# Kernel optimization log

Hardware: AMD Instinct MI355X
Metric: run time of the kernel (lower is better)

The kernel has to match this reference:

```python
import jax, jax.numpy as jnp
import numpy as np

BETA = 0.25  # commitment loss weight (beta)
EPS_NORM = 1e-12  # F.normalize eps


def l2norm(t):
    return t / jnp.clip(jnp.linalg.norm(t, axis=-1, keepdims=True), EPS_NORM)


def setup_inputs() -> dict:
    key = jax.random.key(0)
    k1, k2 = jax.random.split(key)
    z = jax.random.normal(k1, (16, 256, 32, 32), dtype=jnp.float32)
    # EmbeddingEMA with kmeans_init=False: weight = l2norm(randn(n_embed, dim))
    weight = l2norm(jax.random.normal(k2, (8192, 256), dtype=jnp.float32))
    return {"z": z, "weight": weight}


def reference(z, weight):
    # z: [B, C, H, W] -> [B, H, W, C], l2-normalized per token
    zc = l2norm(jnp.transpose(z, (0, 2, 3, 1)))
    B, H, W, D = zc.shape
    zf = zc.reshape(-1, D)  # [N, D]
    zf_d = jax.lax.stop_gradient(zf)
    # negative squared L2 distance: -|z|^2 - |w|^2 + 2 z.w  -> argmax = nearest code
    d = (-jnp.sum(zf_d ** 2, axis=1, keepdims=True)
         - jnp.sum(weight ** 2, axis=1)
         + 2.0 * jnp.einsum('nd,kd->nk', zf_d, weight))  # [N, K]
    idx = jnp.argmax(d, axis=1)  # [N]
    z_q = weight[idx].reshape(B, H, W, D)  # codebook gather
    # commitment loss: beta * mean((sg(z_q) - z)^2)
    loss = BETA * jnp.mean((jax.lax.stop_gradient(z_q) - zc) ** 2)
    # straight-through estimator
    z_q = zc + jax.lax.stop_gradient(z_q - zc)
    z_q = jnp.transpose(z_q, (0, 3, 1, 2))  # back to [B, C, H, W]
    return z_q, loss, idx
```

## Files before the change

kernel.cpp:

```cpp
#include <hip/hip_runtime.h>
#include <math.h>

#define BB   16
#define CC   256
#define HW   1024
#define NN   16384
#define DD   256
#define KK   8192
#define ZQ_SIZE 4194304
#define MARGIN 0.017f
#define GCAP 8192
#define RSPLIT 8

typedef __attribute__((ext_vector_type(8))) short short8;
typedef __attribute__((ext_vector_type(4))) float f32x4;

static __device__ inline unsigned short f2bf(float x) {
    unsigned int u = __float_as_uint(x);
    unsigned int r = (u + 0x7fff + ((u >> 16) & 1)) >> 16;
    return (unsigned short)r;
}

static __device__ inline unsigned long long pack_key(float s, int k) {
    unsigned int bits = __float_as_uint(s);
    unsigned int o = (bits & 0x80000000u) ? ~bits : (bits | 0x80000000u);
    return ((unsigned long long)o << 32) | (unsigned int)(~k);
}

__global__ __launch_bounds__(256) void wsqwb_kernel(const float* __restrict__ W,
                                                    float* __restrict__ wsq,
                                                    unsigned short* __restrict__ wb,
                                                    int* __restrict__ gcnt,
                                                    int* __restrict__ oflow) {
    if (blockIdx.x == 0) {
        gcnt[threadIdx.x] = 0;
        if (threadIdx.x == 0) *oflow = 0;
    }
    {
        const int lane = threadIdx.x & 63;
        const int k = blockIdx.x * 4 + (threadIdx.x >> 6);
        float4 v = *(const float4*)(W + (size_t)k * DD + lane * 4);
        float s = v.x * v.x + v.y * v.y + v.z * v.z + v.w * v.w;
        #pragma unroll
        for (int off = 32; off; off >>= 1) s += __shfl_down(s, off);
        if (lane == 0) wsq[k] = s;
    }
    if (blockIdx.x < 1024) {
        const int ch = blockIdx.x * 256 + threadIdx.x;
        const int c = (ch >> 7) & 7;
        const int r = ch & 127;
        const int kt = ch >> 12, dc = (ch >> 10) & 3;
        const int k = kt * 128 + r;
        const int d0 = dc * 64 + c * 8;
        const float4 v0 = *(const float4*)(W + (size_t)k * DD + d0);
        const float4 v1 = *(const float4*)(W + (size_t)k * DD + d0 + 4);
        uint4 out;
        out.x = (unsigned int)f2bf(v0.x) | ((unsigned int)f2bf(v0.y) << 16);
        out.y = (unsigned int)f2bf(v0.z) | ((unsigned int)f2bf(v0.w) << 16);
        out.z = (unsigned int)f2bf(v1.x) | ((unsigned int)f2bf(v1.y) << 16);
        out.w = (unsigned int)f2bf(v1.z) | ((unsigned int)f2bf(v1.w) << 16);
        *(uint4*)(wb + (size_t)ch * 8) = out;
    }
}

__global__ __launch_bounds__(256) void normalize_kernel(const float* __restrict__ z,
                                                        float* __restrict__ zn,
                                                        float* __restrict__ znsq,
                                                        unsigned short* __restrict__ zb) {
    __shared__ float tile[64][257];
    __shared__ float s_nrm[64];
    const int t   = threadIdx.x;
    const int b   = blockIdx.x >> 4;
    const int hw0 = (blockIdx.x & 15) * 64;

    #pragma unroll
    for (int cg = 0; cg < 16; ++cg) {
        int c  = cg * 16 + (t >> 4);
        int hw = (t & 15) * 4;
        float4 v = *(const float4*)(z + ((size_t)(b * CC + c) << 10) + hw0 + hw);
        tile[hw + 0][c] = v.x;
        tile[hw + 1][c] = v.y;
        tile[hw + 2][c] = v.z;
        tile[hw + 3][c] = v.w;
    }
    __syncthreads();
    if (t < 64) {
        float s = 0.f;
        #pragma unroll 8
        for (int c = 0; c < 256; ++c) { float v = tile[t][c]; s += v * v; }
        float nrm = sqrtf(s);
        nrm = fmaxf(nrm, 1e-12f);
        s_nrm[t] = nrm;
        znsq[(size_t)b * HW + hw0 + t] = s / (nrm * nrm);
    }
    __syncthreads();
    const int n0 = b * HW + hw0;
    for (int r = 0; r < 64; ++r) {
        zn[(size_t)(n0 + r) * DD + t] = tile[r][t] / s_nrm[r];
    }
    const int r    = t & 63;
    const int mt   = n0 >> 7;
    const int rg   = (n0 & 127) + r;
    const float nrm = s_nrm[r];
    #pragma unroll
    for (int loop = 0; loop < 8; ++loop) {
        int comb = loop * 4 + (t >> 6);
        int dc = comb >> 3, c = comb & 7;
        int d0 = dc * 64 + c * 8;
        uint4 out;
        out.x = (unsigned int)f2bf(tile[r][d0 + 0] / nrm) | ((unsigned int)f2bf(tile[r][d0 + 1] / nrm) << 16);
        out.y = (unsigned int)f2bf(tile[r][d0 + 2] / nrm) | ((unsigned int)f2bf(tile[r][d0 + 3] / nrm) << 16);
        out.z = (unsigned int)f2bf(tile[r][d0 + 4] / nrm) | ((unsigned int)f2bf(tile[r][d0 + 5] / nrm) << 16);
        out.w = (unsigned int)f2bf(tile[r][d0 + 6] / nrm) | ((unsigned int)f2bf(tile[r][d0 + 7] / nrm) << 16);
        *(uint4*)(zb + (size_t)(mt * 4 + dc) * 8192 + (size_t)(c * 128 + rg) * 8) = out;
    }
}

__global__ __launch_bounds__(256) void score_kernel(const unsigned short* __restrict__ zb,
                                                    const unsigned short* __restrict__ wb,
                                                    const float* __restrict__ wsqv,
                                                    float* __restrict__ cmax) {
    __shared__ unsigned short sA[8192];
    __shared__ unsigned short sB[8192];
    __shared__ float rowbuf[128][4];
    __shared__ __align__(16) float swsq[128];

    const int tid  = threadIdx.x;
    const int w    = tid >> 6;
    const int lane = tid & 63;
    const int wcr  = w >> 1;
    const int wct  = w & 1;
    const int q    = lane >> 4, c15 = lane & 15;
    const int kt   = blockIdx.x & 63;
    const int mt   = blockIdx.x >> 6;

    if (tid < 128) swsq[tid] = wsqv[kt * 128 + tid];

    f32x4 acc[4][4];
    #pragma unroll
    for (int fi = 0; fi < 4; ++fi)
        #pragma unroll
        for (int fj = 0; fj < 4; ++fj)
            acc[fi][fj] = (f32x4){0.f, 0.f, 0.f, 0.f};

    for (int dc = 0; dc < 4; ++dc) {
        const unsigned short* gA = zb + (size_t)(mt * 4 + dc) * 8192;
        const unsigned short* gB = wb + (size_t)(kt * 4 + dc) * 8192;
        #pragma unroll
        for (int i = 0; i < 4; ++i) {
            int eo = ((w * 4 + i) << 9);
            __builtin_amdgcn_global_load_lds(
                (const __attribute__((address_space(1))) void*)(gA + eo + lane * 8),
                (__attribute__((address_space(3))) void*)(sA + eo), 16, 0, 0);
            __builtin_amdgcn_global_load_lds(
                (const __attribute__((address_space(1))) void*)(gB + eo + lane * 8),
                (__attribute__((address_space(3))) void*)(sB + eo), 16, 0, 0);
        }
        __syncthreads();
        #pragma unroll
        for (int ks = 0; ks < 2; ++ks) {
            short8 tfr[4], cfr[4];
            const int ca = (ks * 4 + q) * 128;
            #pragma unroll
            for (int f = 0; f < 4; ++f) {
                tfr[f] = *(const short8*)(sA + (size_t)(ca + wct * 64 + f * 16 + c15) * 8);
                cfr[f] = *(const short8*)(sB + (size_t)(ca + wcr * 64 + f * 16 + c15) * 8);
            }
            #pragma unroll
            for (int fi = 0; fi < 4; ++fi)
                #pragma unroll
                for (int fj = 0; fj < 4; ++fj)
                    acc[fi][fj] = __builtin_amdgcn_mfma_f32_16x16x32_bf16(
                        cfr[fi], tfr[fj], acc[fi][fj], 0, 0, 0);
        }
        __syncthreads();
    }

    f32x4 wq4[4];
    #pragma unroll
    for (int fi = 0; fi < 4; ++fi)
        wq4[fi] = *(const f32x4*)(&swsq[wcr * 64 + fi * 16 + q * 4]);

    #pragma unroll
    for (int fj = 0; fj < 4; ++fj) {
        float g[2];
        #pragma unroll
        for (int p = 0; p < 2; ++p) {
            float vm = -INFINITY;
            #pragma unroll
            for (int f2 = 0; f2 < 2; ++f2) {
                int fi = p * 2 + f2;
                #pragma unroll
                for (int rg = 0; rg < 4; ++rg)
                    vm = fmaxf(vm, 2.0f * acc[fi][fj][rg] - wq4[fi][rg]);
            }
            vm = fmaxf(vm, __shfl_xor(vm, 16));
            vm = fmaxf(vm, __shfl_xor(vm, 32));
            g[p] = vm;
        }
        if (q == 0) {
            int row = wct * 64 + fj * 16 + c15;
            rowbuf[row][wcr * 2 + 0] = g[0];
            rowbuf[row][wcr * 2 + 1] = g[1];
        }
    }
    __syncthreads();
    {
        int row = tid >> 1, half = tid & 1;
        float2 v2 = make_float2(rowbuf[row][half * 2], rowbuf[row][half * 2 + 1]);
        *(float2*)(cmax + (size_t)(mt * 128 + row) * 256 + kt * 4 + half * 2) = v2;
    }
}

__global__ __launch_bounds__(256) void cand_kernel(const float* __restrict__ cmax,
                                                   unsigned int* __restrict__ gseg,
                                                   int* __restrict__ gcnt,
                                                   unsigned long long* __restrict__ packed,
                                                   int* __restrict__ nflag,
                                                   int* __restrict__ oflow) {
    const int t = threadIdx.x, wv = t >> 6, lane = t & 63;
    const int n = blockIdx.x * 4 + wv;
    float4 c4 = *(const float4*)(cmax + (size_t)n * 256 + lane * 4);
    float lm = fmaxf(fmaxf(c4.x, c4.y), fmaxf(c4.z, c4.w));
    #pragma unroll
    for (int off = 1; off <= 32; off <<= 1) lm = fmaxf(lm, __shfl_xor(lm, off));
    const float thresh = lm - MARGIN;
    if (lane == 0) { packed[n] = 0ull; nflag[n] = 0; }
    float g4[4] = {c4.x, c4.y, c4.z, c4.w};
    #pragma unroll
    for (int j = 0; j < 4; ++j) {
        int g = lane * 4 + j;
        if (g4[j] >= thresh) {
            int pos = atomicAdd(&gcnt[g], 1);
            if (pos < GCAP) gseg[(size_t)g * GCAP + pos] = (unsigned int)n;
            else { nflag[n] = 1; atomicAdd(oflow, 1); }
        }
    }
}

__global__ __launch_bounds__(256) void rescore_kernel(const float* __restrict__ zn,
                                                      const float* __restrict__ W,
                                                      const float* __restrict__ wsqv,
                                                      const float* __restrict__ znsq,
                                                      const unsigned int* __restrict__ gseg,
                                                      const int* __restrict__ gcnt,
                                                      unsigned long long* __restrict__ packed) {
    __shared__ float sW[32 * 260];
    __shared__ float znr[4][2][256];

    const int t = threadIdx.x;
    const int g   = blockIdx.x >> 3;
    const int sub = blockIdx.x & 7;
    int cnt = gcnt[g]; if (cnt > GCAP) cnt = GCAP;
    if (cnt <= sub * 8) return;

    {
        int c = t >> 3, i = t & 7;
        const float4* src = (const float4*)(W + (size_t)g * 8192 + c * 256 + i * 32);
        #pragma unroll
        for (int j = 0; j < 8; ++j)
            *(float4*)(sW + c * 260 + i * 32 + j * 4) = src[j];
    }
    __syncthreads();

    const int wv = t >> 6, lane = t & 63;
    const int h = lane >> 5, c = lane & 31;
    const int k = g * 32 + c;
    const float wq = wsqv[k];
    const float4* wrow = (const float4*)(sW + c * 260);

    for (int base = (sub * 4 + wv) * 2; base < cnt; base += RSPLIT * 8) {
        int idx = base + h; if (idx >= cnt) idx = base;
        int n = (int)gseg[(size_t)g * GCAP + idx];
        *(float4*)(&znr[wv][h][c * 8])     = *(const float4*)(zn + (size_t)n * DD + c * 8);
        *(float4*)(&znr[wv][h][c * 8 + 4]) = *(const float4*)(zn + (size_t)n * DD + c * 8 + 4);
        float d = 0.f;
        #pragma unroll
        for (int j = 0; j < 64; ++j) {
            float4 wv4 = wrow[j];
            float4 zv  = *(const float4*)(&znr[wv][h][j * 4]);
            d += wv4.x * zv.x + wv4.y * zv.y + wv4.z * zv.z + wv4.w * zv.w;
        }
        float s = (-znsq[n] - wq) + 2.0f * d;
        unsigned long long key = pack_key(s, k);
        #pragma unroll
        for (int off = 1; off <= 16; off <<= 1) {
            unsigned long long ok = __shfl_xor(key, off);
            if (ok > key) key = ok;
        }
        if (c == 0) atomicMax(packed + n, key);
    }
}

__global__ __launch_bounds__(256) void fullscan_kernel(const float* __restrict__ zn,
                                                       const float* __restrict__ W,
                                                       const float* __restrict__ wsqv,
                                                       const float* __restrict__ znsq,
                                                       const int* __restrict__ nflag,
                                                       const int* __restrict__ oflow,
                                                       unsigned long long* __restrict__ packed) {
    if (*oflow == 0) return;
    const int t = threadIdx.x, wv = t >> 6, lane = t & 63;
    const int code = lane >> 1, part = lane & 1;
    for (int n = blockIdx.x * 4 + wv; n < NN; n += gridDim.x * 4) {
        if (!nflag[n]) continue;
        float zsq = znsq[n];
        unsigned long long best = 0ull;
        for (int gg = 0; gg < 256; ++gg) {
            int k = gg * 32 + code;
            const float4* wrp = (const float4*)(W + (size_t)k * DD + part * 128);
            const float4* zrp = (const float4*)(zn + (size_t)n * DD + part * 128);
            float d = 0.f;
            #pragma unroll
            for (int jj = 0; jj < 32; ++jj) {
                float4 a = zrp[jj], b = wrp[jj];
                d += a.x * b.x + a.y * b.y + a.z * b.z + a.w * b.w;
            }
            d += __shfl_xor(d, 1);
            unsigned long long key = pack_key((-zsq - wsqv[k]) + 2.0f * d, k);
            if (key > best) best = key;
        }
        #pragma unroll
        for (int off = 1; off <= 32; off <<= 1) {
            unsigned long long ok = __shfl_xor(best, off);
            if (ok > best) best = ok;
        }
        if (lane == 0) atomicMax(packed + n, best);
    }
}

__global__ __launch_bounds__(256) void gatherfin_kernel(const float* __restrict__ W,
                                                        const unsigned long long* __restrict__ packed,
                                                        float* __restrict__ idxf,
                                                        float* __restrict__ partials,
                                                        float* __restrict__ zq) {
    __shared__ int sbk[64];
    const int t   = threadIdx.x;
    const int b   = blockIdx.x >> 4;
    const int hw0 = (blockIdx.x & 15) * 64;
    if (t < 64) {
        int n = b * HW + hw0 + t;
        unsigned long long key = packed[n];
        int k = (int)((~(unsigned int)key) & 0x3FFFu);
        unsigned int o = (unsigned int)(key >> 32);
        unsigned int bits = (o & 0x80000000u) ? (o & 0x7FFFFFFFu) : ~o;
        float s = __uint_as_float(bits);
        sbk[t] = k;
        idxf[n] = (float)k;
        float cc = -s;
        #pragma unroll
        for (int off = 32; off; off >>= 1) cc += __shfl_down(cc, off);
        if (t == 0) partials[blockIdx.x] = cc;
    }
    __syncthreads();
    const int hw  = t & 63;
    const int c0  = (t >> 6) * 4;
    const int row = sbk[hw];
    #pragma unroll
    for (int cg = 0; cg < 16; ++cg) {
        int c = cg * 16 + c0;
        float4 v = *(const float4*)(W + (size_t)row * DD + c);
        size_t base = ((size_t)(b * CC + c) << 10) + hw0 + hw;
        zq[base]        = v.x;
        zq[base + 1024] = v.y;
        zq[base + 2048] = v.z;
        zq[base + 3072] = v.w;
    }
}

__global__ __launch_bounds__(256) void loss_final_kernel(const float* __restrict__ partials,
                                                         float* __restrict__ out_loss) {
    __shared__ float wsum[4];
    const int t = threadIdx.x;
    float v = partials[t];
    #pragma unroll
    for (int off = 32; off; off >>= 1) v += __shfl_down(v, off);
    if ((t & 63) == 0) wsum[t >> 6] = v;
    __syncthreads();
    if (t == 0) {
        float tot = wsum[0] + wsum[1] + wsum[2] + wsum[3];
        *out_loss = 0.25f * (tot / (float)ZQ_SIZE);
    }
}

extern "C" void kernel_launch(void* const* d_in, const int* in_sizes, int n_in,
                              void* d_out, int out_size, void* d_ws, size_t ws_size,
                              hipStream_t stream) {
    const float* z = (const float*)d_in[0];
    const float* W = (const float*)d_in[1];

    float* out   = (float*)d_out;
    float* zq    = out;
    float* loss  = out + ZQ_SIZE;
    float* idxf  = out + ZQ_SIZE + 1;

    float* ws       = (float*)d_ws;
    float* zn       = ws;
    float* znsq     = zn + (size_t)NN * DD;
    float* wsqv     = znsq + NN;
    float* partials = wsqv + KK;
    int*   gcnt     = (int*)(partials + 256);
    int*   oflow    = gcnt + 256;
    int*   nflag    = oflow + 64;
    unsigned short* zb = (unsigned short*)(nflag + NN);
    unsigned short* wb = zb + (size_t)NN * DD;
    float* cmax     = (float*)(wb + (size_t)KK * DD);
    unsigned int* gseg = (unsigned int*)(cmax + (size_t)NN * 256);
    unsigned long long* packed = (unsigned long long*)(gseg + (size_t)256 * GCAP);

    wsqwb_kernel     <<<KK / 4, 256, 0, stream>>>(W, wsqv, wb, gcnt, oflow);
    normalize_kernel <<<BB * 16, 256, 0, stream>>>(z, zn, znsq, zb);
    score_kernel     <<<(NN / 128) * (KK / 128), 256, 0, stream>>>(zb, wb, wsqv, cmax);
    cand_kernel      <<<NN / 4, 256, 0, stream>>>(cmax, gseg, gcnt, packed, nflag, oflow);
    rescore_kernel   <<<256 * RSPLIT, 256, 0, stream>>>(zn, W, wsqv, znsq, gseg, gcnt, packed);
    fullscan_kernel  <<<64, 256, 0, stream>>>(zn, W, wsqv, znsq, nflag, oflow, packed);
    gatherfin_kernel <<<BB * 16, 256, 0, stream>>>(W, packed, idxf, partials, zq);
    loss_final_kernel<<<1, 256, 0, stream>>>(partials, loss);
}
```

Measured before the change: 233.4 us.

## Enlarge score GEMM tiles to 256x256 with double-buffered LDS staging

The bf16 scoring GEMM moves from 128x128 tiles with 256 threads to 256x256 tiles with 512 threads. Loads go through double-buffered global-to-LDS staging, with explicit vmcnt waits so the next d-chunk loads while the current one is computed. MFMA sections are wrapped in barriers and s_setprio. The larger tile halves global reloads of both operands, and the output per block becomes a group max over 32 codes, the same granularity as before. In exchange it uses about 128KB of LDS and more accumulator registers per block, which lowers occupancy.

New measurement: 238.3 us. +2.1%, slower.

```diff
diff --git a/kernel.cpp b/kernel.cpp
--- a/kernel.cpp
+++ b/kernel.cpp
@@ -116,99 +116,130 @@
     }
 }
 
-__global__ __launch_bounds__(256) void score_kernel(const unsigned short* __restrict__ zb,
-                                                    const unsigned short* __restrict__ wb,
-                                                    const float* __restrict__ wsqv,
-                                                    float* __restrict__ cmax) {
-    __shared__ unsigned short sA[8192];
-    __shared__ unsigned short sB[8192];
-    __shared__ float rowbuf[128][4];
-    __shared__ __align__(16) float swsq[128];
+__global__ __launch_bounds__(512, 2) void score_kernel(const unsigned short* __restrict__ zb,
+                                                       const unsigned short* __restrict__ wb,
+                                                       const float* __restrict__ wsqv,
+                                                       float* __restrict__ cmax) {
+    __shared__ __align__(16) unsigned short sT[2][16384];
+    __shared__ __align__(16) unsigned short sC[2][16384];
+    __shared__ float rowbuf[8][260];
+    __shared__ __align__(16) float swsq[256];
 
     const int tid  = threadIdx.x;
     const int w    = tid >> 6;
     const int lane = tid & 63;
-    const int wcr  = w >> 1;
-    const int wct  = w & 1;
+    const int wr   = w >> 2;
+    const int wc   = w & 3;
     const int q    = lane >> 4, c15 = lane & 15;
-    const int kt   = blockIdx.x & 63;
-    const int mt   = blockIdx.x >> 6;
-
-    if (tid < 128) swsq[tid] = wsqv[kt * 128 + tid];
-
-    f32x4 acc[4][4];
-    #pragma unroll
-    for (int fi = 0; fi < 4; ++fi)
+    const int kt   = blockIdx.x & 31;
+    const int mt   = blockIdx.x >> 5;
+    const int mtb  = mt * 8;
+    const int ktb  = kt * 8;
+
+    if (tid < 256) swsq[tid] = wsqv[kt * 256 + tid];
+
+    const int sh = (w >> 1) & 1;
+    auto stage = [&](int bf, int dc) {
+        const unsigned short* gs = (w < 4)
+            ? (zb + (size_t)(mtb + sh * 4 + dc) * 8192)
+            : (wb + (size_t)(ktb + sh * 4 + dc) * 8192);
+        unsigned short* ld = (w < 4) ? &sT[bf][sh * 8192] : &sC[bf][sh * 8192];
+        #pragma unroll
+        for (int i = 0; i < 8; ++i) {
+            const int eo = ((w & 1) * 8 + i) << 9;
+            __builtin_amdgcn_global_load_lds(
+                (const __attribute__((address_space(1))) void*)(gs + eo + lane * 8),
+                (__attribute__((address_space(3))) void*)(ld + eo), 16, 0, 0);
+        }
+    };
+
+    f32x4 acc[8][4];
+    #pragma unroll
+    for (int fi = 0; fi < 8; ++fi)
         #pragma unroll
         for (int fj = 0; fj < 4; ++fj)
             acc[fi][fj] = (f32x4){0.f, 0.f, 0.f, 0.f};
 
-    for (int dc = 0; dc < 4; ++dc) {
-        const unsigned short* gA = zb + (size_t)(mt * 4 + dc) * 8192;
-        const unsigned short* gB = wb + (size_t)(kt * 4 + dc) * 8192;
-        #pragma unroll
-        for (int i = 0; i < 4; ++i) {
-            int eo = ((w * 4 + i) << 9);
-            __builtin_amdgcn_global_load_lds(
-                (const __attribute__((address_space(1))) void*)(gA + eo + lane * 8),
-                (__attribute__((address_space(3))) void*)(sA + eo), 16, 0, 0);
-            __builtin_amdgcn_global_load_lds(
-                (const __attribute__((address_space(1))) void*)(gB + eo + lane * 8),
-                (__attribute__((address_space(3))) void*)(sB + eo), 16, 0, 0);
-        }
-        __syncthreads();
+    const int tHalf = wc >> 1;
+    const int tRow0 = (wc & 1) * 64 + c15;
+
+    stage(0, 0);
+    stage(1, 1);
+    asm volatile("s_waitcnt vmcnt(8)" ::: "memory");
+    __builtin_amdgcn_s_barrier();
+
+    #pragma unroll
+    for (int t = 0; t < 4; ++t) {
+        const int bf = t & 1;
+        const unsigned short* sTb = &sT[bf][tHalf * 8192];
+        const unsigned short* sCb = &sC[bf][wr * 8192];
         #pragma unroll
         for (int ks = 0; ks < 2; ++ks) {
-            short8 tfr[4], cfr[4];
             const int ca = (ks * 4 + q) * 128;
+            short8 tfr[4];
             #pragma unroll
-            for (int f = 0; f < 4; ++f) {
-                tfr[f] = *(const short8*)(sA + (size_t)(ca + wct * 64 + f * 16 + c15) * 8);
-                cfr[f] = *(const short8*)(sB + (size_t)(ca + wcr * 64 + f * 16 + c15) * 8);
+            for (int fj = 0; fj < 4; ++fj)
+                tfr[fj] = *(const short8*)(sTb + (size_t)(ca + tRow0 + fj * 16) * 8);
+            #pragma unroll
+            for (int fih = 0; fih < 2; ++fih) {
+                short8 cfr[4];
+                #pragma unroll
+                for (int f = 0; f < 4; ++f)
+                    cfr[f] = *(const short8*)(sCb + (size_t)(ca + fih * 64 + f * 16 + c15) * 8);
+                __builtin_amdgcn_s_barrier();
+                __builtin_amdgcn_s_setprio(1);
+                #pragma unroll
+                for (int f = 0; f < 4; ++f)
+                    #pragma unroll
+                    for (int fj = 0; fj < 4; ++fj)
+                        acc[fih * 4 + f][fj] = __builtin_amdgcn_mfma_f32_16x16x32_bf16(
+                            cfr[f], tfr[fj], acc[fih * 4 + f][fj], 0, 0, 0);
+                __builtin_amdgcn_s_setprio(0);
+                __builtin_amdgcn_s_barrier();
             }
-            #pragma unroll
-            for (int fi = 0; fi < 4; ++fi)
-                #pragma unroll
-                for (int fj = 0; fj < 4; ++fj)
-                    acc[fi][fj] = __builtin_amdgcn_mfma_f32_16x16x32_bf16(
-                        cfr[fi], tfr[fj], acc[fi][fj], 0, 0, 0);
-        }
-        __syncthreads();
-    }
-
-    f32x4 wq4[4];
-    #pragma unroll
-    for (int fi = 0; fi < 4; ++fi)
-        wq4[fi] = *(const f32x4*)(&swsq[wcr * 64 + fi * 16 + q * 4]);
+        }
+        asm volatile("s_waitcnt lgkmcnt(0)" ::: "memory");
+        __builtin_amdgcn_s_barrier();
+        if (t == 0)      { stage(0, 2); asm volatile("s_waitcnt vmcnt(8)" ::: "memory"); }
+        else if (t == 1) { stage(1, 3); asm volatile("s_waitcnt vmcnt(8)" ::: "memory"); }
+        else if (t == 2) {              asm volatile("s_waitcnt vmcnt(0)" ::: "memory"); }
+        __builtin_amdgcn_s_barrier();
+    }
+
+    f32x4 wq4[8];
+    #pragma unroll
+    for (int fi = 0; fi < 8; ++fi)
+        wq4[fi] = *(const f32x4*)(&swsq[wr * 128 + fi * 16 + q * 4]);
 
     #pragma unroll
     for (int fj = 0; fj < 4; ++fj) {
-        float g[2];
-        #pragma unroll
-        for (int p = 0; p < 2; ++p) {
-            float vm = -INFINITY;
+        float vg[4];
+        #pragma unroll
+        for (int gl = 0; gl < 4; ++gl) {
+            float v = -INFINITY;
             #pragma unroll
             for (int f2 = 0; f2 < 2; ++f2) {
-                int fi = p * 2 + f2;
+                const int fi = gl * 2 + f2;
                 #pragma unroll
                 for (int rg = 0; rg < 4; ++rg)
-                    vm = fmaxf(vm, 2.0f * acc[fi][fj][rg] - wq4[fi][rg]);
+                    v = fmaxf(v, 2.0f * acc[fi][fj][rg] - wq4[fi][rg]);
             }
-            vm = fmaxf(vm, __shfl_xor(vm, 16));
-            vm = fmaxf(vm, __shfl_xor(vm, 32));
-            g[p] = vm;
-        }
-        if (q == 0) {
-            int row = wct * 64 + fj * 16 + c15;
-            rowbuf[row][wcr * 2 + 0] = g[0];
-            rowbuf[row][wcr * 2 + 1] = g[1];
-        }
+            v = fmaxf(v, __shfl_xor(v, 16));
+            v = fmaxf(v, __shfl_xor(v, 32));
+            vg[gl] = v;
+        }
+        const float val = (q == 0) ? vg[0] : (q == 1) ? vg[1] : (q == 2) ? vg[2] : vg[3];
+        rowbuf[wr * 4 + q][wc * 64 + fj * 16 + c15] = val;
     }
     __syncthreads();
     {
-        int row = tid >> 1, half = tid & 1;
-        float2 v2 = make_float2(rowbuf[row][half * 2], rowbuf[row][half * 2 + 1]);
-        *(float2*)(cmax + (size_t)(mt * 128 + row) * 256 + kt * 4 + half * 2) = v2;
+        const int row = tid >> 1, half = tid & 1;
+        float4 o;
+        o.x = rowbuf[half * 4 + 0][row];
+        o.y = rowbuf[half * 4 + 1][row];
+        o.z = rowbuf[half * 4 + 2][row];
+        o.w = rowbuf[half * 4 + 3][row];
+        *(float4*)(cmax + (size_t)(mt * 256 + row) * 256 + kt * 8 + half * 4) = o;
     }
 }
 
@@ -410,7 +441,7 @@
 
     wsqwb_kernel     <<<KK / 4, 256, 0, stream>>>(W, wsqv, wb, gcnt, oflow);
     normalize_kernel <<<BB * 16, 256, 0, stream>>>(z, zn, znsq, zb);
-    score_kernel     <<<(NN / 128) * (KK / 128), 256, 0, stream>>>(zb, wb, wsqv, cmax);
+    score_kernel     <<<(NN / 256) * (KK / 256), 512, 0, stream>>>(zb, wb, wsqv, cmax);
     cand_kernel      <<<NN / 4, 256, 0, stream>>>(cmax, gseg, gcnt, packed, nflag, oflow);
     rescore_kernel   <<<256 * RSPLIT, 256, 0, stream>>>(zn, W, wsqv, znsq, gseg, gcnt, packed);
     fullscan_kernel  <<<64, 256, 0, stream>>>(zn, W, wsqv, znsq, nflag, oflow, packed);
```
